# Kernel optimization log

Measured on AMD Instinct MI355X. Metric: run time of the kernel, lower is better.

## Reference

```python
import jax, jax.numpy as jnp
import numpy as np

HEADS = 12
EMBED_DIM = 768
HEAD_DIM = EMBED_DIM // HEADS
SCALE = HEAD_DIM ** -0.5


def setup_inputs() -> dict:
    key = jax.random.key(0)
    k1, k2, k3 = jax.random.split(key, 3)
    B, N, C = 2, 2048, EMBED_DIM
    x = jax.random.normal(k1, (B, N, C), dtype=jnp.float32)
    # DenseMLP stores weight as (out, in); forward does input @ weight.T (no bias applied)
    W_qkv = jax.random.normal(k2, (3 * C, C), dtype=jnp.float32) * (1.0 / np.sqrt(C))
    W_proj = jax.random.normal(k3, (C, C), dtype=jnp.float32) * (1.0 / np.sqrt(C))
    return {"x": x, "W_qkv": W_qkv, "W_proj": W_proj}


def reference(x, W_qkv, W_proj):
    B, N, C = x.shape
    # qkv projection: (B,N,C) @ (C,3C) -> (B,N,3,H,Dh) -> (3,B,H,N,Dh)
    qkv = jnp.einsum('bnc,oc->bno', x, W_qkv)
    qkv = qkv.reshape(B, N, 3, HEADS, HEAD_DIM).transpose(2, 0, 3, 1, 4)
    q, k, v = qkv[0], qkv[1], qkv[2]
    # eager attention: scores (B,H,N,N), softmax, weighted sum
    attn = jnp.einsum('bhnd,bhmd->bhnm', q, k) * SCALE
    attn = jax.nn.softmax(attn, axis=-1)
    out = jnp.einsum('bhnm,bhmd->bhnd', attn, v)
    out = out.transpose(0, 2, 1, 3).reshape(B, N, C)
    # output projection (bias-free, matching DenseMLP.forward)
    return jnp.einsum('bnc,oc->bno', out, W_proj)
```

## Files before the change

kernel.cpp:

```cpp
#include <hip/hip_runtime.h>


typedef __bf16 bf16;
typedef __attribute__((ext_vector_type(8))) __bf16 bf16x8;
typedef __attribute__((ext_vector_type(4))) __bf16 bf16x4;
typedef __attribute__((ext_vector_type(2))) __bf16 bf16x2;
typedef __attribute__((ext_vector_type(4))) float f32x4;

typedef __attribute__((address_space(1))) void gvoid;
typedef __attribute__((address_space(3))) void lvoid;

__device__ __forceinline__ void gload16(const void* g, void* l) {
  __builtin_amdgcn_global_load_lds((gvoid*)g, (lvoid*)l, 16, 0, 0);
}

__global__ __launch_bounds__(256) void cvt3(const float* __restrict__ x,
                                            const float* __restrict__ wq,
                                            const float* __restrict__ wp,
                                            bf16* __restrict__ xb,
                                            bf16* __restrict__ wqb,
                                            bf16* __restrict__ wpb) {
  const int N1 = 786432, N2 = 442368, N3 = 147456;
  int i = blockIdx.x * 256 + threadIdx.x;
  const int stride = gridDim.x * 256;
  const int total = N1 + N2 + N3;
  for (; i < total; i += stride) {
    const float* src; bf16* dst; int j;
    if (i < N1)           { src = x;  dst = xb;  j = i; }
    else if (i < N1 + N2) { src = wq; dst = wqb; j = i - N1; }
    else                  { src = wp; dst = wpb; j = i - N1 - N2; }
    float4 v = ((const float4*)src)[j];
    bf16x4 o = { (bf16)v.x, (bf16)v.y, (bf16)v.z, (bf16)v.w };
    *(bf16x4*)(dst + (long)j * 4) = o;
  }
}

template <typename OutT, int BM, int BN>
__global__ __launch_bounds__(256, 3) void gemm_nt(const bf16* __restrict__ A,
                                                  const bf16* __restrict__ B,
                                                  OutT* __restrict__ C,
                                                  int K, int lda, int ldb, int ldc,
                                                  int mtiles) {
  constexpr int MI = BM / 32;
  constexpr int NI = BN / 32;
  constexpr int LDSA = BM * 128;
  constexpr int LDSB = BN * 128;
  __shared__ __align__(16) char smem[2 * (LDSA + LDSB)];

  const int tid  = threadIdx.x;
  const int lane = tid & 63;
  const int w    = tid >> 6;
  const int wm   = w >> 1, wn = w & 1;
  const int l15  = lane & 15;
  const int l4   = lane >> 4;
  const int m0   = (blockIdx.x % mtiles) * BM;
  const int n0   = (blockIdx.x / mtiles) * BN;
  const int nt   = K >> 6;

  f32x4 acc[MI][NI] = {};

  auto stage = [&](int buf, int t) {
    const int k0 = t << 6;
    char* sA = smem + buf * (LDSA + LDSB);
    char* sB = sA + LDSA;
#pragma unroll
    for (int i = 0; i < BM * 8 / 256; ++i) {
      const int s = i * 256 + tid;
      const int r = s >> 3;
      const int c = (s & 7) ^ (r & 7);
      gload16(A + (long)(m0 + r) * lda + k0 + c * 8, sA + s * 16);
    }
#pragma unroll
    for (int i = 0; i < BN * 8 / 256; ++i) {
      const int s = i * 256 + tid;
      const int r = s >> 3;
      const int c = (s & 7) ^ (r & 7);
      gload16(B + (long)(n0 + r) * ldb + k0 + c * 8, sB + s * 16);
    }
  };

  auto compute = [&](int buf) {
    const char* sA = smem + buf * (LDSA + LDSB);
    const char* sB = sA + LDSA;
#pragma unroll
    for (int kk = 0; kk < 2; ++kk) {
      bf16x8 a[MI], bb[NI];
#pragma unroll
      for (int mi = 0; mi < MI; ++mi) {
        const int row = wm * (BM / 2) + mi * 16 + l15;
        a[mi] = *(const bf16x8*)(sA + row * 128 + (((kk * 4 + l4) ^ (row & 7)) << 4));
      }
#pragma unroll
      for (int ni = 0; ni < NI; ++ni) {
        const int row = wn * (BN / 2) + ni * 16 + l15;
        bb[ni] = *(const bf16x8*)(sB + row * 128 + (((kk * 4 + l4) ^ (row & 7)) << 4));
      }
#pragma unroll
      for (int mi = 0; mi < MI; ++mi)
#pragma unroll
        for (int ni = 0; ni < NI; ++ni)
          acc[mi][ni] = __builtin_amdgcn_mfma_f32_16x16x32_bf16(a[mi], bb[ni], acc[mi][ni], 0, 0, 0);
    }
  };

  stage(0, 0);
  __syncthreads();
  for (int t = 0; t < nt; ++t) {
    if (t + 1 < nt) stage((t + 1) & 1, t + 1);
    compute(t & 1);
    __syncthreads();
  }

#pragma unroll
  for (int mi = 0; mi < MI; ++mi)
#pragma unroll
    for (int ni = 0; ni < NI; ++ni)
#pragma unroll
      for (int r = 0; r < 4; ++r) {
        const int row = m0 + wm * (BM / 2) + mi * 16 + l4 * 4 + r;
        const int col = n0 + wn * (BN / 2) + ni * 16 + l15;
        C[(long)row * ldc + col] = (OutT)acc[mi][ni][r];
      }
}

__global__ __launch_bounds__(256, 3) void attn_fwd(const bf16* __restrict__ qkv,
                                                   bf16* __restrict__ O) {
  __shared__ __align__(16) char Ks[16384];
  __shared__ __align__(16) char Vs[16384];
  const int tid  = threadIdx.x;
  const int lane = tid & 63;
  const int w    = tid >> 6;
  const int l15  = lane & 15;
  const int l4   = lane >> 4;
  const int b    = blockIdx.y / 12;
  const int h    = blockIdx.y % 12;
  const int q0   = blockIdx.x * 64;
  const unsigned base = (unsigned)b * 2048u * 2304u;
  const int h64  = h * 64;
  const unsigned VSTEP = 64u * 2304u;

  bf16x8 qf[2];
  {
    const bf16* qp = qkv + base + (unsigned)(q0 + w * 16 + l15) * 2304u + h64 + l4 * 8;
#pragma unroll
    for (int kk = 0; kk < 2; ++kk) {
      bf16x8 t = *(const bf16x8*)(qp + kk * 32);
#pragma unroll
      for (int j = 0; j < 8; ++j) qf[kk][j] = (bf16)((float)t[j] * 0.18033688f);
    }
  }

  const int krow0 = tid >> 3;
  const int kc0   = (tid & 7) ^ (krow0 & 7);
  const int krow1 = (256 + tid) >> 3;
  const int kc1   = (tid & 7) ^ (krow1 & 7);
  unsigned koff0 = base + (unsigned)krow0 * 2304u + 768u + h64 + kc0 * 8;
  unsigned koff1 = base + (unsigned)krow1 * 2304u + 768u + h64 + kc1 * 8;

  auto k_stage = [&](int buf) {
    gload16(qkv + koff0, Ks + buf * 8192 + tid * 16);
    gload16(qkv + koff1, Ks + buf * 8192 + 4096 + tid * 16);
    koff0 += VSTEP;
    koff1 += VSTEP;
  };

  const int p    = tid & 31;
  const int dblk = tid >> 5;
  const int pc   = p >> 2;
  const int cw   = (p & 3) * 4;
  unsigned voff = base + (unsigned)(2 * p) * 2304u + 1536u + h64 + dblk * 8;

  auto vt_write = [&](char* W, const bf16x8& r0, const bf16x8& r1) {
#pragma unroll
    for (int j = 0; j < 8; ++j) {
      const int d = dblk * 8 + j;
      bf16x2 t2 = { r0[j], r1[j] };
      *(bf16x2*)(W + d * 128 + ((pc ^ j) << 4) + cw) = t2;
    }
  };

  float m = -1e30f, lsum = 0.f;
  f32x4 o[4] = {};

  k_stage(0);
  {
    bf16x8 r0 = *(const bf16x8*)(qkv + voff);
    bf16x8 r1 = *(const bf16x8*)(qkv + voff + 2304);
    voff += VSTEP;
    vt_write(Vs, r0, r1);
  }
  __syncthreads();

  for (int t = 0; t < 32; ++t) {
    const int buf = t & 1;
    const bool pre = (t < 31);

    bf16x8 nr0, nr1;
    if (pre) {
      k_stage(buf ^ 1);
      nr0 = *(const bf16x8*)(qkv + voff);
      nr1 = *(const bf16x8*)(qkv + voff + 2304);
      voff += VSTEP;
    }

    const char* Kb = Ks + buf * 8192;
    f32x4 s[4];
    __builtin_amdgcn_s_setprio(1);
#pragma unroll
    for (int f = 0; f < 4; ++f) {
      const int row = f * 16 + l15;
      const char* krow = Kb + row * 128;
      bf16x8 k0 = *(const bf16x8*)(krow + (((0 + l4) ^ (row & 7)) << 4));
      bf16x8 k1 = *(const bf16x8*)(krow + (((4 + l4) ^ (row & 7)) << 4));
      f32x4 acc = {};
      acc = __builtin_amdgcn_mfma_f32_16x16x32_bf16(k0, qf[0], acc, 0, 0, 0);
      acc = __builtin_amdgcn_mfma_f32_16x16x32_bf16(k1, qf[1], acc, 0, 0, 0);
      s[f] = acc;
    }
    __builtin_amdgcn_s_setprio(0);

    float tm = s[0][0];
#pragma unroll
    for (int f = 0; f < 4; ++f)
#pragma unroll
      for (int r = 0; r < 4; ++r) tm = fmaxf(tm, s[f][r]);

    if (__any(tm > m + 8.f)) {
      tm = fmaxf(tm, __shfl_xor(tm, 16));
      tm = fmaxf(tm, __shfl_xor(tm, 32));
      const float mn = fmaxf(m, tm);
      const float alpha = __builtin_amdgcn_exp2f(m - mn);
      m = mn;
      lsum *= alpha;
      f32x4 av;
#pragma unroll
      for (int r = 0; r < 4; ++r) av[r] = __shfl(alpha, l4 * 4 + r);
#pragma unroll
      for (int fd = 0; fd < 4; ++fd) o[fd] *= av;
    }

    float rs = 0.f;
#pragma unroll
    for (int f = 0; f < 4; ++f)
#pragma unroll
      for (int r = 0; r < 4; ++r) {
        const float pv = __builtin_amdgcn_exp2f(s[f][r] - m);
        s[f][r] = pv;
        rs += pv;
      }
    lsum += rs;

    bf16x8 pa[2];
#pragma unroll
    for (int kk = 0; kk < 2; ++kk)
#pragma unroll
      for (int j = 0; j < 8; ++j)
        pa[kk][j] = (bf16)s[kk * 2 + (j >> 2)][j & 3];

    const char* Vb = Vs + buf * 8192;
    const int sub = (l4 & 1) * 8;
    __builtin_amdgcn_s_setprio(1);
#pragma unroll
    for (int kk = 0; kk < 2; ++kk) {
      const int cr0 = kk * 4 + (l4 >> 1);
#pragma unroll
      for (int fd = 0; fd < 4; ++fd) {
        const int d = fd * 16 + l15;
        const char* row = Vb + d * 128;
        bf16x4 lo = *(const bf16x4*)(row + ((cr0 ^ (d & 7)) << 4) + sub);
        bf16x4 hi = *(const bf16x4*)(row + (((cr0 + 2) ^ (d & 7)) << 4) + sub);
        bf16x8 vb = __builtin_shufflevector(lo, hi, 0, 1, 2, 3, 4, 5, 6, 7);
        o[fd] = __builtin_amdgcn_mfma_f32_16x16x32_bf16(pa[kk], vb, o[fd], 0, 0, 0);
      }
    }
    __builtin_amdgcn_s_setprio(0);

    if (pre) vt_write(Vs + (buf ^ 1) * 8192, nr0, nr1);

    __syncthreads();
  }

  lsum += __shfl_xor(lsum, 16);
  lsum += __shfl_xor(lsum, 32);

  const float inv = 1.0f / lsum;
  f32x4 iv;
#pragma unroll
  for (int r = 0; r < 4; ++r) iv[r] = __shfl(inv, l4 * 4 + r);
  bf16* op = O + ((long)(b * 2048 + q0 + w * 16 + l4 * 4)) * 768 + h64 + l15;
#pragma unroll
  for (int fd = 0; fd < 4; ++fd)
#pragma unroll
    for (int r = 0; r < 4; ++r)
      op[(long)r * 768 + fd * 16] = (bf16)(o[fd][r] * iv[r]);
}

extern "C" void kernel_launch(void* const* d_in, const int* in_sizes, int n_in,
                              void* d_out, int out_size, void* d_ws, size_t ws_size,
                              hipStream_t stream) {
  const float* x  = (const float*)d_in[0];
  const float* wq = (const float*)d_in[1];
  const float* wp = (const float*)d_in[2];
  float* out = (float*)d_out;
  char* ws = (char*)d_ws;

  bf16* xb   = (bf16*)(ws + 0);
  bf16* wqb  = (bf16*)(ws + 6291456);
  bf16* wpb  = (bf16*)(ws + 9830400);
  bf16* qkvb = (bf16*)(ws + 11010048);
  bf16* ob   = (bf16*)(ws + 29884416);

  cvt3<<<dim3(1024), dim3(256), 0, stream>>>(x, wq, wp, xb, wqb, wpb);
  gemm_nt<bf16, 64, 128><<<dim3(64 * 18), dim3(256), 0, stream>>>(
      xb, wqb, qkvb, 768, 768, 768, 2304, 64);
  attn_fwd<<<dim3(32, 24), dim3(256), 0, stream>>>(qkvb, ob);
  gemm_nt<float, 64, 64><<<dim3(64 * 12), dim3(256), 0, stream>>>(
      ob, wpb, out, 768, 768, 768, 768, 64);
}
```

Baseline: 154.4 us.

## Split attention KV range across two blocks and merge partials with LSE weights

After: 162.1 us. +5.0%, slower.

```diff
diff --git a/kernel.cpp b/kernel.cpp
--- a/kernel.cpp
+++ b/kernel.cpp
@@ -123,25 +123,29 @@
       }
 }
 
-__global__ __launch_bounds__(256, 3) void attn_fwd(const bf16* __restrict__ qkv,
-                                                   bf16* __restrict__ O) {
+__global__ __launch_bounds__(256, 5) void attn_fwd(const bf16* __restrict__ qkv,
+                                                   bf16* __restrict__ ob,
+                                                   bf16* __restrict__ pb1,
+                                                   float* __restrict__ wbuf) {
   __shared__ __align__(16) char Ks[16384];
   __shared__ __align__(16) char Vs[16384];
   const int tid  = threadIdx.x;
   const int lane = tid & 63;
-  const int w    = tid >> 6;
+  const int wv   = tid >> 6;
   const int l15  = lane & 15;
   const int l4   = lane >> 4;
   const int b    = blockIdx.y / 12;
   const int h    = blockIdx.y % 12;
+  const int z    = blockIdx.z;
   const int q0   = blockIdx.x * 64;
   const unsigned base = (unsigned)b * 2048u * 2304u;
   const int h64  = h * 64;
   const unsigned VSTEP = 64u * 2304u;
+  const unsigned kvoff = (unsigned)(z * 1024) * 2304u;
 
   bf16x8 qf[2];
   {
-    const bf16* qp = qkv + base + (unsigned)(q0 + w * 16 + l15) * 2304u + h64 + l4 * 8;
+    const bf16* qp = qkv + base + (unsigned)(q0 + wv * 16 + l15) * 2304u + h64 + l4 * 8;
 #pragma unroll
     for (int kk = 0; kk < 2; ++kk) {
       bf16x8 t = *(const bf16x8*)(qp + kk * 32);
@@ -154,8 +158,8 @@
   const int kc0   = (tid & 7) ^ (krow0 & 7);
   const int krow1 = (256 + tid) >> 3;
   const int kc1   = (tid & 7) ^ (krow1 & 7);
-  unsigned koff0 = base + (unsigned)krow0 * 2304u + 768u + h64 + kc0 * 8;
-  unsigned koff1 = base + (unsigned)krow1 * 2304u + 768u + h64 + kc1 * 8;
+  unsigned koff0 = base + kvoff + (unsigned)krow0 * 2304u + 768u + h64 + kc0 * 8;
+  unsigned koff1 = base + kvoff + (unsigned)krow1 * 2304u + 768u + h64 + kc1 * 8;
 
   auto k_stage = [&](int buf) {
     gload16(qkv + koff0, Ks + buf * 8192 + tid * 16);
@@ -168,7 +172,7 @@
   const int dblk = tid >> 5;
   const int pc   = p >> 2;
   const int cw   = (p & 3) * 4;
-  unsigned voff = base + (unsigned)(2 * p) * 2304u + 1536u + h64 + dblk * 8;
+  unsigned voff = base + kvoff + (unsigned)(2 * p) * 2304u + 1536u + h64 + dblk * 8;
 
   auto vt_write = [&](char* W, const bf16x8& r0, const bf16x8& r1) {
 #pragma unroll
@@ -191,9 +195,9 @@
   }
   __syncthreads();
 
-  for (int t = 0; t < 32; ++t) {
+  for (int t = 0; t < 16; ++t) {
     const int buf = t & 1;
-    const bool pre = (t < 31);
+    const bool pre = (t < 15);
 
     bf16x8 nr0, nr1;
     if (pre) {
@@ -283,16 +287,53 @@
   lsum += __shfl_xor(lsum, 16);
   lsum += __shfl_xor(lsum, 32);
 
+  if (l4 == 0) {
+    const int token = b * 2048 + q0 + wv * 16 + l15;
+    wbuf[(z * 4096 + token) * 12 + h] = m + __log2f(lsum);
+  }
+
   const float inv = 1.0f / lsum;
   f32x4 iv;
 #pragma unroll
   for (int r = 0; r < 4; ++r) iv[r] = __shfl(inv, l4 * 4 + r);
-  bf16* op = O + ((long)(b * 2048 + q0 + w * 16 + l4 * 4)) * 768 + h64 + l15;
+  bf16* dst = z ? pb1 : ob;
+  bf16* op = dst + ((long)(b * 2048 + q0 + wv * 16 + l4 * 4)) * 768 + h64 + l15;
 #pragma unroll
   for (int fd = 0; fd < 4; ++fd)
 #pragma unroll
     for (int r = 0; r < 4; ++r)
       op[(long)r * 768 + fd * 16] = (bf16)(o[fd][r] * iv[r]);
+}
+
+__global__ __launch_bounds__(256) void attn_merge(bf16* __restrict__ ob,
+                                                  const bf16* __restrict__ pb1,
+                                                  const float* __restrict__ wbuf) {
+  const int b   = blockIdx.y / 12;
+  const int h   = blockIdx.y % 12;
+  const int q0  = blockIdx.x * 64;
+  const int row = threadIdx.x >> 2;
+  const int ds  = (threadIdx.x & 3) * 16;
+  const int token = b * 2048 + q0 + row;
+
+  const float w0 = wbuf[token * 12 + h];
+  const float w1 = wbuf[(4096 + token) * 12 + h];
+  const float M  = fmaxf(w0, w1);
+  const float e0 = __builtin_amdgcn_exp2f(w0 - M);
+  const float e1 = __builtin_amdgcn_exp2f(w1 - M);
+  const float inv = 1.0f / (e0 + e1);
+  const float f0 = e0 * inv, f1 = e1 * inv;
+
+  bf16* po = ob + (long)token * 768 + h * 64 + ds;
+  const bf16* pp = pb1 + (long)token * 768 + h * 64 + ds;
+#pragma unroll
+  for (int half = 0; half < 2; ++half) {
+    bf16x8 a = *(const bf16x8*)(po + half * 8);
+    bf16x8 c = *(const bf16x8*)(pp + half * 8);
+    bf16x8 r;
+#pragma unroll
+    for (int j = 0; j < 8; ++j) r[j] = (bf16)(f0 * (float)a[j] + f1 * (float)c[j]);
+    *(bf16x8*)(po + half * 8) = r;
+  }
 }
 
 extern "C" void kernel_launch(void* const* d_in, const int* in_sizes, int n_in,
@@ -309,11 +350,14 @@
   bf16* wpb  = (bf16*)(ws + 9830400);
   bf16* qkvb = (bf16*)(ws + 11010048);
   bf16* ob   = (bf16*)(ws + 29884416);
+  bf16*  pb1  = (bf16*)(ws + 0);
+  float* wbuf = (float*)(ws + 6291456);
 
   cvt3<<<dim3(1024), dim3(256), 0, stream>>>(x, wq, wp, xb, wqb, wpb);
   gemm_nt<bf16, 64, 128><<<dim3(64 * 18), dim3(256), 0, stream>>>(
       xb, wqb, qkvb, 768, 768, 768, 2304, 64);
-  attn_fwd<<<dim3(32, 24), dim3(256), 0, stream>>>(qkvb, ob);
+  attn_fwd<<<dim3(32, 24, 2), dim3(256), 0, stream>>>(qkvb, ob, pb1, wbuf);
+  attn_merge<<<dim3(32, 24), dim3(256), 0, stream>>>(ob, pb1, wbuf);
   gemm_nt<float, 64, 64><<<dim3(64 * 12), dim3(256), 0, stream>>>(
       ob, wpb, out, 768, 768, 768, 768, 64);
 }
```
